# Performance work log

Hardware: AMD Instinct MI355X
Metric: run time of the kernel (lower is better)

## Reference

```python
import jax, jax.numpy as jnp
import numpy as np

N = 100800          # anchors for YOLOv5 @ 1280px: 3*(160^2+80^2+40^2)
NC = 80             # COCO classes
CONF_THRES = 0.4
IOU_THRES = 0.45
MAX_DET = 1000
MAX_NMS = 4096      # candidate cap before IoU (ultralytics uses 30000; reduced for KxK IoU memory)
MAX_WH = 7680.0     # per-class box offset (agnostic=False)


def setup_inputs() -> dict:
    key = jax.random.key(0)
    k1, k2, k3, k4 = jax.random.split(key, 4)
    xy = jax.random.uniform(k1, (1, N, 2), jnp.float32) * 1280.0   # box centers
    wh = jax.random.uniform(k2, (1, N, 2), jnp.float32) * 200.0 + 2.0  # box sizes
    obj = jax.random.uniform(k3, (1, N, 1), jnp.float32)           # objectness
    cls = jax.random.uniform(k4, (1, N, NC), jnp.float32)          # class scores
    pred = jnp.concatenate([xy, wh, obj, cls], axis=-1)            # [1, N, 85]
    return {"pred": pred}


def _xywh2xyxy(b):
    xy, wh = b[:, :2], b[:, 2:4]
    return jnp.concatenate([xy - wh * 0.5, xy + wh * 0.5], axis=-1)


def _nms(pred):
    p = pred[0]                                   # [N, 85] (module returns image 0)
    cls_conf = p[:, 5:] * p[:, 4:5]               # conf = obj * cls
    conf = jnp.max(cls_conf, axis=-1)             # best-class confidence [N]
    cls = jnp.argmax(cls_conf, axis=-1)           # best-class index [N]
    box = _xywh2xyxy(p[:, :4])                    # [N, 4] xyxy

    # candidate filter (conf > thres) + cap to top MAX_NMS by confidence
    scores = jnp.where(conf > CONF_THRES, conf, -jnp.inf)
    top_s, idx = jax.lax.top_k(scores, MAX_NMS)   # sorted descending
    b = box[idx]                                  # [K, 4]
    c = cls[idx]                                  # [K]
    valid = top_s > CONF_THRES                    # [K]

    # per-class NMS: offset boxes by class index so classes never overlap
    ob = b + (c.astype(b.dtype) * MAX_WH)[:, None]
    area = (ob[:, 2] - ob[:, 0]) * (ob[:, 3] - ob[:, 1])
    lt = jnp.maximum(ob[:, None, :2], ob[None, :, :2])
    rb = jnp.minimum(ob[:, None, 2:], ob[None, :, 2:])
    whi = jnp.clip(rb - lt, 0.0)
    inter = whi[..., 0] * whi[..., 1]             # [K, K]
    iou = inter / (area[:, None] + area[None, :] - inter + 1e-9)

    # greedy NMS: box j is suppressed if a kept, higher-scoring box i overlaps it
    upper = jnp.triu(jnp.ones((MAX_NMS, MAX_NMS), bool), 1)
    sup_mat = jax.lax.stop_gradient((iou > IOU_THRES) & upper)

    def body(i, keep):
        return keep & ~(sup_mat[i] & keep[i])

    keep = jax.lax.stop_gradient(jax.lax.fori_loop(0, MAX_NMS, body, valid))

    # top max_det kept detections, padded with zeros -> fixed [MAX_DET, 6]
    fscore = jnp.where(keep, top_s, -jnp.inf)
    fs, fi = jax.lax.top_k(fscore, MAX_DET)
    out = jnp.concatenate(
        [b[fi], top_s[fi][:, None], c[fi].astype(b.dtype)[:, None]], axis=-1
    )                                             # [MAX_DET, 6] = x1,y1,x2,y2,conf,cls
    return jnp.where((fs > CONF_THRES)[:, None], out, 0.0)


def reference(pred):
    return _nms(pred)
```

## Files before the change

kernel.cpp:

```cpp
#include <hip/hip_runtime.h>
#include <stdint.h>

#pragma clang fp contract(off)

#define N_ANCH 100800
#define ROWLEN 85
#define NCLS 80
#define CONF_T 0.4f
#define IOU_T 0.45f
#define MAXNMS 4096
#define MAXDET 1000
#define NBINS 4096
#define MAX_WH_F 7680.0f
#define SROWS 132
#define SCORE_BLKS ((N_ANCH + SROWS - 1) / SROWS)
#define POISON32 0xAAAAAAAAu


__device__ __forceinline__ unsigned long long aload64(const unsigned long long* p) {
  return __hip_atomic_load(p, __ATOMIC_RELAXED, __HIP_MEMORY_SCOPE_AGENT);
}
__device__ __forceinline__ void astore64(unsigned long long* p, unsigned long long v) {
  __hip_atomic_store(p, v, __ATOMIC_RELAXED, __HIP_MEMORY_SCOPE_AGENT);
}
__device__ __forceinline__ unsigned aload32(const unsigned* p) {
  return __hip_atomic_load(p, __ATOMIC_RELAXED, __HIP_MEMORY_SCOPE_AGENT);
}
__device__ __forceinline__ void astore32(unsigned* p, unsigned v) {
  __hip_atomic_store(p, v, __ATOMIC_RELAXED, __HIP_MEMORY_SCOPE_AGENT);
}

__global__ __launch_bounds__(256) void score_kernel(
    const float* __restrict__ pred, float* __restrict__ confArr,
    unsigned char* __restrict__ clsArr, unsigned short* __restrict__ binArr,
    unsigned* __restrict__ hist, unsigned* __restrict__ base,
    unsigned* __restrict__ meta) {
  __shared__ float s[SROWS * ROWLEN];
  __shared__ unsigned s_scan[4];
  __shared__ unsigned s_last;
  const int tid = threadIdx.x;
  const int wid = tid >> 6, lane = tid & 63;

  {
    const float4* p4 = (const float4*)pred;
    float4* s4 = (float4*)s;
    const int NV = SROWS * ROWLEN / 4;
    const size_t g0 = (size_t)blockIdx.x * NV;
    const size_t gmax = (size_t)N_ANCH * ROWLEN / 4;
    for (int v = tid; v < NV; v += 256) {
      size_t g = g0 + v;
      if (g < gmax) s4[v] = p4[g];
    }
  }
  __syncthreads();

  if (tid < SROWS) {
    int n = blockIdx.x * SROWS + tid;
    if (n < N_ANCH) {
      const float* row = s + tid * ROWLEN;
      float obj = row[4];
      float best = row[5] * obj;
      int bc = 0;
      for (int i = 1; i < NCLS; ++i) {
        float v = row[5 + i] * obj;
        if (v > best) { best = v; bc = i; }
      }
      confArr[n] = best;
      clsArr[n] = (unsigned char)bc;
      unsigned short bo = 0;
      if (best > CONF_T) {
        int b = (int)(best * 4096.0f);
        if (b > NBINS - 1) b = NBINS - 1;
        bo = (unsigned short)b;
        atomicAdd(&hist[b], 1u);
      }
      binArr[n] = bo;
    }
  }

  __syncthreads();
  if (tid == 0) {
    unsigned ret = __hip_atomic_fetch_add(&meta[8], 1u, __ATOMIC_RELAXED,
                                          __HIP_MEMORY_SCOPE_AGENT);
    s_last = (ret == POISON32 + (unsigned)(SCORE_BLKS - 1)) ? 1u : 0u;
  }
  __syncthreads();
  if (s_last == 0) return;

  unsigned hv[16];
  unsigned ssum = 0;
#pragma unroll
  for (int k = 0; k < 16; ++k) {
    hv[k] = aload32(&hist[NBINS - 1 - (tid * 16 + k)]) - POISON32;
    ssum += hv[k];
  }
  unsigned incl = ssum;
  for (int d = 1; d < 64; d <<= 1) {
    unsigned v = __shfl_up(incl, d);
    if (lane >= d) incl += v;
  }
  if (lane == 63) s_scan[wid] = incl;
  __syncthreads();
  if (tid == 0) {
    unsigned acc = 0;
    for (int w = 0; w < 4; ++w) { unsigned t = s_scan[w]; s_scan[w] = acc; acc += t; }
  }
  __syncthreads();
  unsigned e = s_scan[wid] + (incl - ssum);
#pragma unroll
  for (int k = 0; k < 16; ++k) {
    int b = NBINS - 1 - (tid * 16 + k);
    base[b] = e;
    if (e <= (unsigned)MAXNMS && e + hv[k] > (unsigned)MAXNMS) {
      meta[0] = (unsigned)(b + 1);
      meta[1] = e;
    }
    e += hv[k];
  }
  if (tid == 255) meta[2] = e;
}

__global__ __launch_bounds__(256) void gather_kernel(
    const float* __restrict__ confArr, const unsigned short* __restrict__ binArr,
    const unsigned* __restrict__ base, unsigned* __restrict__ cnt,
    const unsigned* __restrict__ meta, unsigned long long* __restrict__ cand) {
  int v = blockIdx.x * 256 + threadIdx.x;
  if (v >= N_ANCH / 4) return;
  ushort4 b4 = ((const ushort4*)binArr)[v];
  const unsigned Bcut = meta[0];
  int n0 = v * 4;
#pragma unroll
  for (int k = 0; k < 4; ++k) {
    unsigned b = (k == 0) ? b4.x : (k == 1) ? b4.y : (k == 2) ? b4.z : b4.w;
    if (b && b >= Bcut) {
      int n = n0 + k;
      unsigned r = atomicAdd(&cnt[b], 1u) - POISON32;
      cand[base[b] + r] =
          ((unsigned long long)__float_as_uint(confArr[n]) << 32) |
          (unsigned long long)(~(unsigned)n);
    }
  }
}

__global__ __launch_bounds__(256) void class_kernel(
    const float* __restrict__ pred, const unsigned char* __restrict__ clsArr,
    const unsigned* __restrict__ base, const unsigned* __restrict__ cnt,
    unsigned* __restrict__ meta, const unsigned long long* __restrict__ cand,
    unsigned* __restrict__ keep32, unsigned long long* __restrict__ sortedKey,
    float* __restrict__ out) {
  __shared__ unsigned long long s_cand[MAXNMS];
  __shared__ unsigned long long s_mkey[128];
  __shared__ unsigned s_mslot[128];
  __shared__ float4 s_obox[128];
  __shared__ unsigned long long s_okey[128];
  __shared__ unsigned s_oslot[128];
  __shared__ unsigned s_K;
  __shared__ unsigned s_scan[4];
  __shared__ unsigned s_last;
  __shared__ unsigned short s_kept[MAXDET];
  __shared__ unsigned s_tot;

  const int tid = threadIdx.x;
  const int wid = tid >> 6, lane = tid & 63;
  const int c = blockIdx.x;

  const unsigned Bcut = meta[0];
  const unsigned total =
      Bcut ? meta[1] : (meta[2] > (unsigned)MAXNMS ? (unsigned)MAXNMS : meta[2]);

  if (tid == 0) s_K = 0;
  {
    const ulonglong2* c2 = (const ulonglong2*)cand;
    for (int v = tid; v < MAXNMS / 2; v += 256) {
      ulonglong2 kk = c2[v];
      int i0 = v * 2, i1 = i0 + 1;
      s_cand[i0] = (i0 < (int)total) ? kk.x : 0ull;
      s_cand[i1] = (i1 < (int)total) ? kk.y : 0ull;
    }
  }
  __syncthreads();

  for (int i = tid; i < (int)total; i += 256) {
    unsigned long long key = s_cand[i];
    unsigned a = ~(unsigned)key;
    if (clsArr[a] == (unsigned char)c) {
      float conf = __uint_as_float((unsigned)(key >> 32));
      int b = (int)(conf * 4096.0f);
      if (b > NBINS - 1) b = NBINS - 1;
      unsigned bs = base[b], ct = cnt[b] - POISON32;
      unsigned r = 0;
      for (unsigned j = 0; j < ct; ++j) r += (s_cand[bs + j] > key) ? 1u : 0u;
      unsigned slot = bs + r;
      unsigned idx = atomicAdd(&s_K, 1u);
      if (idx < 128) { s_mkey[idx] = key; s_mslot[idx] = slot; }
    }
  }
  __syncthreads();
  int K = (int)s_K;
  if (K > 128) K = 128;
  if (K > 0) {
    if (tid < K) {
      unsigned myslot = s_mslot[tid];
      unsigned ord = 0;
      for (int j = 0; j < K; ++j) ord += (s_mslot[j] < myslot) ? 1u : 0u;
      unsigned long long key = s_mkey[tid];
      unsigned a = ~(unsigned)key;
      const float* row = pred + (size_t)a * ROWLEN;
      float bx = row[0], by = row[1], bw = row[2], bh = row[3];
      float x1 = bx - bw * 0.5f, y1 = by - bh * 0.5f;
      float x2 = bx + bw * 0.5f, y2 = by + bh * 0.5f;
      float off = (float)c * MAX_WH_F;
      s_obox[ord] = make_float4(x1 + off, y1 + off, x2 + off, y2 + off);
      s_okey[ord] = key;
      s_oslot[ord] = myslot;
    }
    __syncthreads();
    if (wid == 0) {
      const int nch = (K + 63) >> 6;
      float ox1[2], oy1[2], ox2[2], oy2[2];
#pragma unroll
      for (int q = 0; q < 2; ++q) {
        ox1[q] = oy1[q] = ox2[q] = oy2[q] = 0.f;
        int j = q * 64 + lane;
        if (q < nch && j < K) {
          float4 bb = s_obox[j];
          ox1[q] = bb.x; oy1[q] = bb.y; ox2[q] = bb.z; oy2[q] = bb.w;
        }
      }
      unsigned long long cm00 = 0ull, cm01 = 0ull, cm10 = 0ull, cm11 = 0ull;
#pragma unroll
      for (int qi = 0; qi < 2; ++qi) {
        if (qi < nch) {
          int lim = K - qi * 64; if (lim > 64) lim = 64;
          for (int li = 0; li < lim; ++li) {
            float bx1 = __shfl(qi ? ox1[1] : ox1[0], li);
            float by1 = __shfl(qi ? oy1[1] : oy1[0], li);
            float bx2 = __shfl(qi ? ox2[1] : ox2[0], li);
            float by2 = __shfl(qi ? oy2[1] : oy2[0], li);
            float areai = (bx2 - bx1) * (by2 - by1);
            int i = qi * 64 + li;
            unsigned long long bit = (1ull << li);
#pragma unroll
            for (int q = 0; q < 2; ++q) {
              if (q < nch) {
                int j = q * 64 + lane;
                float ltx = fmaxf(bx1, ox1[q]);
                float lty = fmaxf(by1, oy1[q]);
                float rbx = fminf(bx2, ox2[q]);
                float rby = fminf(by2, oy2[q]);
                float iw = fmaxf(rbx - ltx, 0.f);
                float ih = fmaxf(rby - lty, 0.f);
                float inter = iw * ih;
                float areaj = (ox2[q] - ox1[q]) * (oy2[q] - oy1[q]);
                float iou = inter / (areai + areaj - inter + 1e-9f);
                bool sup = (iou > IOU_T) && (i < j) && (j < K);
                if (sup) {
                  if (q == 0) { if (qi == 0) cm00 |= bit; else cm01 |= bit; }
                  else       { if (qi == 0) cm10 |= bit; else cm11 |= bit; }
                }
              }
            }
          }
        }
      }
      unsigned long long vm0, vm1, km0, km1;
      {
        int r0 = K;      vm0 = (r0 >= 64) ? ~0ull : ((1ull << r0) - 1ull);
        int r1 = K - 64; vm1 = (r1 >= 64) ? ~0ull
                                          : ((r1 <= 0) ? 0ull : ((1ull << r1) - 1ull));
        km0 = vm0; km1 = vm1;
      }
      for (int it = 0; it < 200; ++it) {
        unsigned long long s0 = cm00 & km0;
        if (nch > 1) s0 |= cm01 & km1;
        unsigned long long b0 = __ballot(s0 == 0ull) & vm0;
        unsigned long long b1 = km1;
        if (nch > 1) {
          unsigned long long s1 = (cm10 & km0) | (cm11 & km1);
          b1 = __ballot(s1 == 0ull) & vm1;
        }
        bool same = (b0 == km0) && (b1 == km1);
        km0 = b0; km1 = b1;
        if (same) break;
      }
#pragma unroll
      for (int q = 0; q < 2; ++q) {
        int j = q * 64 + lane;
        if (q < nch && j < K) {
          unsigned slot = s_oslot[j];
          astore32(&keep32[slot],
                   (unsigned)(((q == 0 ? km0 : km1) >> lane) & 1ull));
          astore64(&sortedKey[slot], s_okey[j]);
        }
      }
    }
  }

  __syncthreads();
  if (tid == 0) {
    unsigned ret = __hip_atomic_fetch_add(&meta[9], 1u, __ATOMIC_RELAXED,
                                          __HIP_MEMORY_SCOPE_AGENT);
    s_last = (ret == POISON32 + (unsigned)(NCLS - 1)) ? 1u : 0u;
  }
  __syncthreads();
  if (s_last == 0) return;

  unsigned flags[16];
  unsigned fsum = 0;
#pragma unroll
  for (int k = 0; k < 16; ++k) {
    flags[k] = (aload32(&keep32[tid * 16 + k]) == 1u) ? 1u : 0u;
    fsum += flags[k];
  }
  unsigned incl = fsum;
  for (int d = 1; d < 64; d <<= 1) {
    unsigned v = __shfl_up(incl, d);
    if (lane >= d) incl += v;
  }
  if (lane == 63) s_scan[wid] = incl;
  __syncthreads();
  if (tid == 0) {
    unsigned acc = 0;
    for (int w = 0; w < 4; ++w) { unsigned t = s_scan[w]; s_scan[w] = acc; acc += t; }
    s_tot = acc;
  }
  __syncthreads();
  unsigned rank = s_scan[wid] + (incl - fsum);
#pragma unroll
  for (int k = 0; k < 16; ++k) {
    if (flags[k]) {
      if (rank < MAXDET) s_kept[rank] = (unsigned short)(tid * 16 + k);
      rank++;
    }
  }
  __syncthreads();
  unsigned tot = s_tot;
  for (int r = tid; r < MAXDET; r += 256) {
    float* o = out + (size_t)r * 6;
    if (r < (int)tot) {
      int slot = s_kept[r];
      unsigned long long key = aload64(&sortedKey[slot]);
      unsigned a = ~(unsigned)key;
      float conf = __uint_as_float((unsigned)(key >> 32));
      const float* row = pred + (size_t)a * ROWLEN;
      float bx = row[0], by = row[1], bw = row[2], bh = row[3];
      o[0] = bx - bw * 0.5f; o[1] = by - bh * 0.5f;
      o[2] = bx + bw * 0.5f; o[3] = by + bh * 0.5f;
      o[4] = conf; o[5] = (float)clsArr[a];
    } else {
      o[0] = 0.f; o[1] = 0.f; o[2] = 0.f;
      o[3] = 0.f; o[4] = 0.f; o[5] = 0.f;
    }
  }
}

extern "C" void kernel_launch(void* const* d_in, const int* in_sizes, int n_in,
                              void* d_out, int out_size, void* d_ws, size_t ws_size,
                              hipStream_t stream) {
  (void)in_sizes; (void)n_in; (void)out_size; (void)ws_size;
  const float* pred = (const float*)d_in[0];
  float* out = (float*)d_out;
  char* ws = (char*)d_ws;

  unsigned* hist = (unsigned*)(ws + 0);
  unsigned* cnt = (unsigned*)(ws + 16384);
  unsigned* keep32 = (unsigned*)(ws + 32768);
  unsigned* meta = (unsigned*)(ws + 49152);
  unsigned* base = (unsigned*)(ws + 49280);
  unsigned long long* cand = (unsigned long long*)(ws + 65664);
  unsigned long long* sortedKey = (unsigned long long*)(ws + 98432);
  float* confArr = (float*)(ws + 131200);
  unsigned char* clsArr = (unsigned char*)(ws + 534400);
  unsigned short* binArr = (unsigned short*)(ws + 635200);


  score_kernel<<<SCORE_BLKS, 256, 0, stream>>>(pred, confArr, clsArr, binArr,
                                               hist, base, meta);
  gather_kernel<<<(N_ANCH / 4 + 255) / 256, 256, 0, stream>>>(
      confArr, binArr, base, cnt, meta, cand);
  class_kernel<<<NCLS, 256, 0, stream>>>(pred, clsArr, base, cnt, meta, cand,
                                         keep32, sortedKey, out);
}
```

Before: 128.5 us.

## Fuse candidate gather into per-class kernel and sort only kept detections

Removes the separate gather kernel and its global candidate array. Each of the 80 class blocks now scans all anchor bins directly and collects its own class's candidates. Kept boxes are appended compactly to a global list through a wave-aggregated atomic. The last block then bucket-sorts only the kept keys in shared memory to produce the output. This saves one launch and the global scatter/rank work, but every class block now reads the full bin and class arrays (about 100K entries each), which adds redundant memory traffic.

```diff
diff --git a/kernel.cpp b/kernel.cpp
--- a/kernel.cpp
+++ b/kernel.cpp
@@ -26,15 +26,11 @@
 __device__ __forceinline__ unsigned aload32(const unsigned* p) {
   return __hip_atomic_load(p, __ATOMIC_RELAXED, __HIP_MEMORY_SCOPE_AGENT);
 }
-__device__ __forceinline__ void astore32(unsigned* p, unsigned v) {
-  __hip_atomic_store(p, v, __ATOMIC_RELAXED, __HIP_MEMORY_SCOPE_AGENT);
-}
 
 __global__ __launch_bounds__(256) void score_kernel(
     const float* __restrict__ pred, float* __restrict__ confArr,
     unsigned char* __restrict__ clsArr, unsigned short* __restrict__ binArr,
-    unsigned* __restrict__ hist, unsigned* __restrict__ base,
-    unsigned* __restrict__ meta) {
+    unsigned* __restrict__ hist, unsigned* __restrict__ meta) {
   __shared__ float s[SROWS * ROWLEN];
   __shared__ unsigned s_scan[4];
   __shared__ unsigned s_last;
@@ -110,111 +106,72 @@
 #pragma unroll
   for (int k = 0; k < 16; ++k) {
     int b = NBINS - 1 - (tid * 16 + k);
-    base[b] = e;
-    if (e <= (unsigned)MAXNMS && e + hv[k] > (unsigned)MAXNMS) {
+    if (e <= (unsigned)MAXNMS && e + hv[k] > (unsigned)MAXNMS)
       meta[0] = (unsigned)(b + 1);
-      meta[1] = e;
-    }
     e += hv[k];
   }
-  if (tid == 255) meta[2] = e;
-}
-
-__global__ __launch_bounds__(256) void gather_kernel(
-    const float* __restrict__ confArr, const unsigned short* __restrict__ binArr,
-    const unsigned* __restrict__ base, unsigned* __restrict__ cnt,
-    const unsigned* __restrict__ meta, unsigned long long* __restrict__ cand) {
-  int v = blockIdx.x * 256 + threadIdx.x;
-  if (v >= N_ANCH / 4) return;
-  ushort4 b4 = ((const ushort4*)binArr)[v];
-  const unsigned Bcut = meta[0];
-  int n0 = v * 4;
-#pragma unroll
-  for (int k = 0; k < 4; ++k) {
-    unsigned b = (k == 0) ? b4.x : (k == 1) ? b4.y : (k == 2) ? b4.z : b4.w;
-    if (b && b >= Bcut) {
-      int n = n0 + k;
-      unsigned r = atomicAdd(&cnt[b], 1u) - POISON32;
-      cand[base[b] + r] =
-          ((unsigned long long)__float_as_uint(confArr[n]) << 32) |
-          (unsigned long long)(~(unsigned)n);
-    }
-  }
 }
 
 __global__ __launch_bounds__(256) void class_kernel(
-    const float* __restrict__ pred, const unsigned char* __restrict__ clsArr,
-    const unsigned* __restrict__ base, const unsigned* __restrict__ cnt,
-    unsigned* __restrict__ meta, const unsigned long long* __restrict__ cand,
-    unsigned* __restrict__ keep32, unsigned long long* __restrict__ sortedKey,
-    float* __restrict__ out) {
-  __shared__ unsigned long long s_cand[MAXNMS];
+    const float* __restrict__ pred, const float* __restrict__ confArr,
+    const unsigned char* __restrict__ clsArr,
+    const unsigned short* __restrict__ binArr, unsigned* __restrict__ meta,
+    unsigned long long* __restrict__ keptKeys, float* __restrict__ out) {
   __shared__ unsigned long long s_mkey[128];
-  __shared__ unsigned s_mslot[128];
+  __shared__ unsigned long long s_okey[128];
   __shared__ float4 s_obox[128];
-  __shared__ unsigned long long s_okey[128];
-  __shared__ unsigned s_oslot[128];
   __shared__ unsigned s_K;
   __shared__ unsigned s_scan[4];
   __shared__ unsigned s_last;
-  __shared__ unsigned short s_kept[MAXDET];
-  __shared__ unsigned s_tot;
+  __shared__ unsigned long long s_sorted[MAXNMS];
+  __shared__ unsigned s_cnt2[NBINS];
+  __shared__ unsigned s_cur[NBINS];
 
   const int tid = threadIdx.x;
   const int wid = tid >> 6, lane = tid & 63;
   const int c = blockIdx.x;
-
   const unsigned Bcut = meta[0];
-  const unsigned total =
-      Bcut ? meta[1] : (meta[2] > (unsigned)MAXNMS ? (unsigned)MAXNMS : meta[2]);
 
   if (tid == 0) s_K = 0;
-  {
-    const ulonglong2* c2 = (const ulonglong2*)cand;
-    for (int v = tid; v < MAXNMS / 2; v += 256) {
-      ulonglong2 kk = c2[v];
-      int i0 = v * 2, i1 = i0 + 1;
-      s_cand[i0] = (i0 < (int)total) ? kk.x : 0ull;
-      s_cand[i1] = (i1 < (int)total) ? kk.y : 0ull;
-    }
-  }
-  __syncthreads();
-
-  for (int i = tid; i < (int)total; i += 256) {
-    unsigned long long key = s_cand[i];
-    unsigned a = ~(unsigned)key;
-    if (clsArr[a] == (unsigned char)c) {
-      float conf = __uint_as_float((unsigned)(key >> 32));
-      int b = (int)(conf * 4096.0f);
-      if (b > NBINS - 1) b = NBINS - 1;
-      unsigned bs = base[b], ct = cnt[b] - POISON32;
-      unsigned r = 0;
-      for (unsigned j = 0; j < ct; ++j) r += (s_cand[bs + j] > key) ? 1u : 0u;
-      unsigned slot = bs + r;
-      unsigned idx = atomicAdd(&s_K, 1u);
-      if (idx < 128) { s_mkey[idx] = key; s_mslot[idx] = slot; }
+  __syncthreads();
+  for (int v = tid; v < N_ANCH / 4; v += 256) {
+    ushort4 b4 = ((const ushort4*)binArr)[v];
+    int n0 = v * 4;
+#pragma unroll
+    for (int k = 0; k < 4; ++k) {
+      unsigned b = (k == 0) ? b4.x : (k == 1) ? b4.y : (k == 2) ? b4.z : b4.w;
+      if (b && b >= Bcut) {
+        int n = n0 + k;
+        if (clsArr[n] == (unsigned char)c) {
+          unsigned idx = atomicAdd(&s_K, 1u);
+          if (idx < 128)
+            s_mkey[idx] =
+                ((unsigned long long)__float_as_uint(confArr[n]) << 32) |
+                (unsigned long long)(~(unsigned)n);
+        }
+      }
     }
   }
   __syncthreads();
   int K = (int)s_K;
   if (K > 128) K = 128;
+
   if (K > 0) {
     if (tid < K) {
-      unsigned myslot = s_mslot[tid];
+      unsigned long long key = s_mkey[tid];
       unsigned ord = 0;
-      for (int j = 0; j < K; ++j) ord += (s_mslot[j] < myslot) ? 1u : 0u;
-      unsigned long long key = s_mkey[tid];
+      for (int j = 0; j < K; ++j) ord += (s_mkey[j] > key) ? 1u : 0u;
       unsigned a = ~(unsigned)key;
       const float* row = pred + (size_t)a * ROWLEN;
       float bx = row[0], by = row[1], bw = row[2], bh = row[3];
       float x1 = bx - bw * 0.5f, y1 = by - bh * 0.5f;
       float x2 = bx + bw * 0.5f, y2 = by + bh * 0.5f;
       float off = (float)c * MAX_WH_F;
+      s_okey[ord] = key;
       s_obox[ord] = make_float4(x1 + off, y1 + off, x2 + off, y2 + off);
-      s_okey[ord] = key;
-      s_oslot[ord] = myslot;
     }
     __syncthreads();
+
     if (wid == 0) {
       const int nch = (K + 63) >> 6;
       float ox1[2], oy1[2], ox2[2], oy2[2];
@@ -286,11 +243,22 @@
 #pragma unroll
       for (int q = 0; q < 2; ++q) {
         int j = q * 64 + lane;
-        if (q < nch && j < K) {
-          unsigned slot = s_oslot[j];
-          astore32(&keep32[slot],
-                   (unsigned)(((q == 0 ? km0 : km1) >> lane) & 1ull));
-          astore64(&sortedKey[slot], s_okey[j]);
+        bool kp = (q < nch && j < K) &&
+                  ((((q == 0) ? km0 : km1) >> lane) & 1ull);
+        unsigned long long m = __ballot(kp);
+        if (m != 0ull) {
+          unsigned basep = 0;
+          if (lane == 0)
+            basep = __hip_atomic_fetch_add(&meta[11],
+                                           (unsigned)__popcll(m),
+                                           __ATOMIC_RELAXED,
+                                           __HIP_MEMORY_SCOPE_AGENT);
+          basep = __shfl(basep, 0);
+          if (kp) {
+            unsigned pos = (basep - POISON32) +
+                           (unsigned)__popcll(m & ((1ull << lane) - 1ull));
+            if (pos < (unsigned)MAXNMS) astore64(&keptKeys[pos], s_okey[j]);
+          }
         }
       }
     }
@@ -305,52 +273,84 @@
   __syncthreads();
   if (s_last == 0) return;
 
-  unsigned flags[16];
-  unsigned fsum = 0;
-#pragma unroll
-  for (int k = 0; k < 16; ++k) {
-    flags[k] = (aload32(&keep32[tid * 16 + k]) == 1u) ? 1u : 0u;
-    fsum += flags[k];
-  }
-  unsigned incl = fsum;
-  for (int d = 1; d < 64; d <<= 1) {
-    unsigned v = __shfl_up(incl, d);
-    if (lane >= d) incl += v;
-  }
-  if (lane == 63) s_scan[wid] = incl;
-  __syncthreads();
-  if (tid == 0) {
-    unsigned acc = 0;
-    for (int w = 0; w < 4; ++w) { unsigned t = s_scan[w]; s_scan[w] = acc; acc += t; }
-    s_tot = acc;
-  }
-  __syncthreads();
-  unsigned rank = s_scan[wid] + (incl - fsum);
-#pragma unroll
-  for (int k = 0; k < 16; ++k) {
-    if (flags[k]) {
-      if (rank < MAXDET) s_kept[rank] = (unsigned short)(tid * 16 + k);
-      rank++;
-    }
-  }
-  __syncthreads();
-  unsigned tot = s_tot;
-  for (int r = tid; r < MAXDET; r += 256) {
-    float* o = out + (size_t)r * 6;
-    if (r < (int)tot) {
-      int slot = s_kept[r];
-      unsigned long long key = aload64(&sortedKey[slot]);
+  unsigned tot = aload32(&meta[11]) - POISON32;
+  if (tot > (unsigned)MAXNMS) tot = (unsigned)MAXNMS;
+
+#pragma unroll
+  for (int k = 0; k < 16; ++k) s_cnt2[tid * 16 + k] = 0;
+  __syncthreads();
+
+  for (unsigned i = tid; i < tot; i += 256) {
+    unsigned long long key = aload64(&keptKeys[i]);
+    float conf = __uint_as_float((unsigned)(key >> 32));
+    int b = (int)(conf * 4096.0f);
+    if (b > NBINS - 1) b = NBINS - 1;
+    atomicAdd(&s_cnt2[b], 1u);
+  }
+  __syncthreads();
+
+  {
+    unsigned hv[16];
+    unsigned ssum = 0;
+#pragma unroll
+    for (int k = 0; k < 16; ++k) {
+      hv[k] = s_cnt2[NBINS - 1 - (tid * 16 + k)];
+      ssum += hv[k];
+    }
+    unsigned incl = ssum;
+    for (int d = 1; d < 64; d <<= 1) {
+      unsigned v = __shfl_up(incl, d);
+      if (lane >= d) incl += v;
+    }
+    if (lane == 63) s_scan[wid] = incl;
+    __syncthreads();
+    if (tid == 0) {
+      unsigned acc = 0;
+      for (int w = 0; w < 4; ++w) { unsigned t = s_scan[w]; s_scan[w] = acc; acc += t; }
+    }
+    __syncthreads();
+    unsigned e = s_scan[wid] + (incl - ssum);
+#pragma unroll
+    for (int k = 0; k < 16; ++k) {
+      int b = NBINS - 1 - (tid * 16 + k);
+      s_cur[b] = e;
+      e += hv[k];
+    }
+  }
+  __syncthreads();
+
+  for (unsigned i = tid; i < tot; i += 256) {
+    unsigned long long key = aload64(&keptKeys[i]);
+    float conf = __uint_as_float((unsigned)(key >> 32));
+    int b = (int)(conf * 4096.0f);
+    if (b > NBINS - 1) b = NBINS - 1;
+    unsigned pos = atomicAdd(&s_cur[b], 1u);
+    s_sorted[pos] = key;
+  }
+  __syncthreads();
+
+  for (unsigned i = tid; i < tot; i += 256) {
+    unsigned long long key = s_sorted[i];
+    float conf = __uint_as_float((unsigned)(key >> 32));
+    int b = (int)(conf * 4096.0f);
+    if (b > NBINS - 1) b = NBINS - 1;
+    unsigned end = s_cur[b], start = end - s_cnt2[b];
+    unsigned r = start;
+    for (unsigned j = start; j < end; ++j) r += (s_sorted[j] > key) ? 1u : 0u;
+    if (r < (unsigned)MAXDET) {
       unsigned a = ~(unsigned)key;
-      float conf = __uint_as_float((unsigned)(key >> 32));
       const float* row = pred + (size_t)a * ROWLEN;
       float bx = row[0], by = row[1], bw = row[2], bh = row[3];
+      float* o = out + (size_t)r * 6;
       o[0] = bx - bw * 0.5f; o[1] = by - bh * 0.5f;
       o[2] = bx + bw * 0.5f; o[3] = by + bh * 0.5f;
       o[4] = conf; o[5] = (float)clsArr[a];
-    } else {
-      o[0] = 0.f; o[1] = 0.f; o[2] = 0.f;
-      o[3] = 0.f; o[4] = 0.f; o[5] = 0.f;
-    }
+    }
+  }
+  for (unsigned r = tot + tid; r < (unsigned)MAXDET; r += 256) {
+    float* o = out + (size_t)r * 6;
+    o[0] = 0.f; o[1] = 0.f; o[2] = 0.f;
+    o[3] = 0.f; o[4] = 0.f; o[5] = 0.f;
   }
 }
 
@@ -363,21 +363,15 @@
   char* ws = (char*)d_ws;
 
   unsigned* hist = (unsigned*)(ws + 0);
-  unsigned* cnt = (unsigned*)(ws + 16384);
-  unsigned* keep32 = (unsigned*)(ws + 32768);
-  unsigned* meta = (unsigned*)(ws + 49152);
-  unsigned* base = (unsigned*)(ws + 49280);
-  unsigned long long* cand = (unsigned long long*)(ws + 65664);
-  unsigned long long* sortedKey = (unsigned long long*)(ws + 98432);
-  float* confArr = (float*)(ws + 131200);
-  unsigned char* clsArr = (unsigned char*)(ws + 534400);
-  unsigned short* binArr = (unsigned short*)(ws + 635200);
+  unsigned* meta = (unsigned*)(ws + 16384);
+  unsigned long long* keptKeys = (unsigned long long*)(ws + 16512);
+  float* confArr = (float*)(ws + 49280);
+  unsigned char* clsArr = (unsigned char*)(ws + 452480);
+  unsigned short* binArr = (unsigned short*)(ws + 553280);
 
 
   score_kernel<<<SCORE_BLKS, 256, 0, stream>>>(pred, confArr, clsArr, binArr,
-                                               hist, base, meta);
-  gather_kernel<<<(N_ANCH / 4 + 255) / 256, 256, 0, stream>>>(
-      confArr, binArr, base, cnt, meta, cand);
-  class_kernel<<<NCLS, 256, 0, stream>>>(pred, clsArr, base, cnt, meta, cand,
-                                         keep32, sortedKey, out);
-}
+                                               hist, meta);
+  class_kernel<<<NCLS, 256, 0, stream>>>(pred, confArr, clsArr, binArr, meta,
+                                         keptKeys, out);
+}
```

Result: slower. 209.5 us (+63.1%).
